# Kernel optimization log

Hardware: AMD Instinct MI355X
Metric: run time of the kernel (lower is better)

The kernel has to match this reference:

```python
import jax, jax.numpy as jnp
import numpy as np
import math

CH, CTX, NH, G = 512, 768, 8, 32
EPS = 1e-5

def setup_inputs() -> dict:
    key = jax.random.key(0)
    ks = jax.random.split(key, 12)
    s = 0.02
    return {
        "x": jax.random.normal(ks[0], (1, CH, 64, 64), dtype=jnp.float32),
        "context": jax.random.normal(ks[1], (1, CTX, 64, 64), dtype=jnp.float32),
        "gn_w": jnp.ones((CH,), jnp.float32),
        "gn_b": jnp.zeros((CH,), jnp.float32),
        "wq": jax.random.normal(ks[2], (CH, CH), jnp.float32) * s,
        "bq": jnp.zeros((CH,), jnp.float32),
        "wk": jax.random.normal(ks[3], (CH, CTX), jnp.float32) * s,
        "bk": jnp.zeros((CH,), jnp.float32),
        "wv": jax.random.normal(ks[4], (CH, CTX), jnp.float32) * s,
        "bv": jnp.zeros((CH,), jnp.float32),
        "wo": jax.random.normal(ks[5], (CH, CH), jnp.float32) * s,
        "bo": jnp.zeros((CH,), jnp.float32),
    }

def _group_norm(x, w, b):
    B, C, H, W = x.shape
    r = x.reshape(B, G, C // G, H, W)
    mu = jnp.mean(r, axis=(2, 3, 4), keepdims=True)
    var = jnp.var(r, axis=(2, 3, 4), keepdims=True)
    r = (r - mu) * jax.lax.rsqrt(var + EPS)
    return r.reshape(B, C, H, W) * w[None, :, None, None] + b[None, :, None, None]

def _conv1x1(x, w, b):
    # x: [B,Cin,H,W], w: [Cout,Cin]
    return jnp.einsum('bchw,oc->bohw', x, w) + b[None, :, None, None]

def reference(x, context, gn_w, gn_b, wq, bq, wk, bk, wv, bv, wo, bo):
    B, C, H, W = x.shape
    residual = x
    h = _group_norm(x, gn_w, gn_b)
    q = _conv1x1(h, wq, bq).reshape(B, NH, C // NH, H * W)
    k = _conv1x1(context, wk, bk).reshape(B, NH, C // NH, H * W)
    v = _conv1x1(context, wv, bv).reshape(B, NH, C // NH, H * W)
    scale = 1.0 / math.sqrt(C // NH)
    # chunked softmax in the original is mathematically exact full softmax
    attn = jnp.einsum('bhdi,bhdj->bhij', q, k) * scale
    attn = jax.nn.softmax(attn, axis=-1)
    out = jnp.einsum('bhij,bhdj->bhdi', attn, v).reshape(B, C, H, W)
    out = _conv1x1(out, wo, bo)
    return out + residual
```

## Files before the change

kernel.cpp:

```cpp
#include <hip/hip_runtime.h>
#include <cstdint>
#include <cstddef>

typedef __attribute__((ext_vector_type(8))) short bf16x8;
typedef __attribute__((ext_vector_type(4))) float f32x4;
typedef unsigned short u16;

#define QSCALE (0.125f * 1.44269504088896f)

__device__ inline u16 f2bf(float x) {
  uint32_t u = __builtin_bit_cast(uint32_t, x);
  u += 0x7FFFu + ((u >> 16) & 1u);
  return (u16)(u >> 16);
}
__device__ inline float bf2f(u16 v) {
  return __builtin_bit_cast(float, (uint32_t)v << 16);
}
__device__ inline uint32_t cvtpk(float a, float b) {
  uint32_t r;
  asm("v_cvt_pk_bf16_f32 %0, %1, %2" : "=v"(r) : "v"(a), "v"(b));
  return r;
}
__device__ inline float exp2raw(float x) {
  float r;
  asm("v_exp_f32 %0, %1" : "=v"(r) : "v"(x));
  return r;
}
__device__ inline void gload_lds16(const void* g, void* l) {
  __builtin_amdgcn_global_load_lds(
      (const __attribute__((address_space(1))) char*)g,
      (__attribute__((address_space(3))) char*)l, 16, 0, 0);
}

__global__ __launch_bounds__(256) void gn_partial(const float* __restrict__ x,
                                                  float* __restrict__ gsum,
                                                  float* __restrict__ gsum2) {
  __shared__ float rs[4], rss[4];
  int b = blockIdx.x;
  int g = b >> 3, sl = b & 7;
  const float* base = x + (size_t)g * 65536 + sl * 8192;
  int t = threadIdx.x;
  float s = 0.f, ss = 0.f;
#pragma unroll
  for (int i = 0; i < 8; ++i) {
    float4 v = *reinterpret_cast<const float4*>(base + i * 1024 + t * 4);
    s += v.x + v.y + v.z + v.w;
    ss += v.x * v.x + v.y * v.y + v.z * v.z + v.w * v.w;
  }
  for (int d = 32; d; d >>= 1) {
    s += __shfl_down(s, d, 64);
    ss += __shfl_down(ss, d, 64);
  }
  int wid = t >> 6;
  if ((t & 63) == 0) { rs[wid] = s; rss[wid] = ss; }
  __syncthreads();
  if (t == 0) {
    atomicAdd(gsum + g, rs[0] + rs[1] + rs[2] + rs[3]);
    atomicAdd(gsum2 + g, rss[0] + rss[1] + rss[2] + rss[3]);
  }
}

__global__ __launch_bounds__(256) void prep(const float* __restrict__ wq, u16* __restrict__ wqB,
                                            const float* __restrict__ wk, u16* __restrict__ wkB,
                                            const float* __restrict__ wv, u16* __restrict__ wvB,
                                            const float* __restrict__ wo, u16* __restrict__ woB,
                                            const float* __restrict__ x, u16* __restrict__ hT,
                                            const float* __restrict__ ctx, u16* __restrict__ ctxT,
                                            const float* __restrict__ gnw, const float* __restrict__ gnb,
                                            const float* __restrict__ gsum, const float* __restrict__ gsum2) {
  int b = blockIdx.x;
  int t = threadIdx.x;
  if (b < 1280) {
    const float* s; u16* d; int off;
    if (b < 256)       { s = wq; d = wqB; off = b; }
    else if (b < 640)  { s = wk; d = wkB; off = b - 256; }
    else if (b < 1024) { s = wv; d = wvB; off = b - 640; }
    else               { s = wo; d = woB; off = b - 1024; }
    int i = (off * 256 + t) * 4;
    float4 v = *reinterpret_cast<const float4*>(s + i);
    u16 o[4] = {f2bf(v.x), f2bf(v.y), f2bf(v.z), f2bf(v.w)};
    *reinterpret_cast<uint2*>(d + i) = *reinterpret_cast<const uint2*>(o);
    return;
  }
  __shared__ float tile[64][65];
  const float* in; u16* out; int C, p0, c0;
  bool norm = false;
  if (b < 1792) {
    int idx = b - 1280;
    in = x; out = hT; C = 512; p0 = (idx & 63) * 64; c0 = (idx >> 6) * 64; norm = true;
  } else {
    int idx = b - 1792;
    in = ctx; out = ctxT; C = 768; p0 = (idx & 63) * 64; c0 = (idx >> 6) * 64;
  }
  int cl = t >> 4, pl = (t & 15) * 4;
#pragma unroll
  for (int rep = 0; rep < 4; ++rep) {
    int c = cl + rep * 16;
    float4 v = *reinterpret_cast<const float4*>(in + (size_t)(c0 + c) * 4096 + p0 + pl);
    float s = 1.f, f = 0.f;
    if (norm) {
      int g = (c0 + c) >> 4;
      float mu = gsum[g] * (1.f / 65536.f);
      float var = gsum2[g] * (1.f / 65536.f) - mu * mu;
      float rstd = rsqrtf(var + 1e-5f);
      s = gnw[c0 + c] * rstd;
      f = gnb[c0 + c] - mu * s;
    }
    tile[c][pl + 0] = v.x * s + f;
    tile[c][pl + 1] = v.y * s + f;
    tile[c][pl + 2] = v.z * s + f;
    tile[c][pl + 3] = v.w * s + f;
  }
  __syncthreads();
#pragma unroll
  for (int rep = 0; rep < 16; ++rep) {
    int idx = rep * 256 + t;
    int pw = idx >> 6, cw = idx & 63;
    out[(size_t)(p0 + pw) * C + c0 + cw] = f2bf(tile[cw][pw]);
  }
}

template <int BIAS_MODE, bool OUT_BF16, bool ADD_RES>
__device__ inline void gemm_body(u16* __restrict__ aT, u16* __restrict__ bT,
                                 const u16* __restrict__ A, const u16* __restrict__ B,
                                 void* __restrict__ Dv,
                                 const float* __restrict__ bias,
                                 const float* __restrict__ res,
                                 int Rb, int K, float oscale, int bx, int by) {
  const int t = threadIdx.x;
  const int lane = t & 63, w = t >> 6;
  const int wr = w >> 1, wc = w & 1;
  const int l15 = lane & 15, l4 = lane >> 4;
  const int i0 = by * 128, j0 = bx * 64;
  const int r_st = t >> 3, slot = t & 7;
  f32x4 acc[4][2] = {};

  auto stage = [&](int kt, int b) {
#pragma unroll
    for (int q = 0; q < 4; ++q) {
      int row = q * 32 + r_st;
      int koff = kt + ((slot ^ (row & 7)) * 8);
      gload_lds16(A + (size_t)(i0 + row) * K + koff, (char*)aT + b * 16384 + q * 4096 + w * 1024);
    }
#pragma unroll
    for (int q = 0; q < 2; ++q) {
      int row = q * 32 + r_st;
      int koff = kt + ((slot ^ (row & 7)) * 8);
      gload_lds16(B + (size_t)(j0 + row) * K + koff, (char*)bT + b * 8192 + q * 4096 + w * 1024);
    }
  };

  const int nt = K / 64;
  stage(0, 0);
  stage(64, 1);

  for (int tt = 0; tt < nt; ++tt) {
    const int cur = tt % 3;
    if (tt + 1 < nt) asm volatile("s_waitcnt vmcnt(6)\n\ts_barrier" ::: "memory");
    else             asm volatile("s_waitcnt vmcnt(0)\n\ts_barrier" ::: "memory");
    if (tt + 2 < nt) stage((tt + 2) * 64, (tt + 2) % 3);

#pragma unroll
    for (int kk = 0; kk < 2; ++kk) {
      bf16x8 af[4], bfr[2];
#pragma unroll
      for (int m = 0; m < 4; ++m) {
        int row = wr * 64 + m * 16 + l15;
        int off = row * 128 + ((l4 * 16 + kk * 64) ^ ((row & 7) << 4));
        af[m] = *reinterpret_cast<const bf16x8*>((const char*)aT + cur * 16384 + off);
      }
#pragma unroll
      for (int n = 0; n < 2; ++n) {
        int row = wc * 32 + n * 16 + l15;
        int off = row * 128 + ((l4 * 16 + kk * 64) ^ ((row & 7) << 4));
        bfr[n] = *reinterpret_cast<const bf16x8*>((const char*)bT + cur * 8192 + off);
      }
#pragma unroll
      for (int m = 0; m < 4; ++m)
#pragma unroll
        for (int n = 0; n < 2; ++n)
          acc[m][n] = __builtin_amdgcn_mfma_f32_16x16x32_bf16(af[m], bfr[n], acc[m][n], 0, 0, 0);
    }
  }

#pragma unroll
  for (int m = 0; m < 4; ++m) {
    int ib = i0 + wr * 64 + m * 16 + l4 * 4;
#pragma unroll
    for (int n = 0; n < 2; ++n) {
      int j = j0 + wc * 32 + n * 16 + l15;
#pragma unroll
      for (int r = 0; r < 4; ++r) {
        int i = ib + r;
        float v = acc[m][n][r];
        if (BIAS_MODE == 0) v += bias[i];
        else v += bias[j];
        v *= oscale;
        if (ADD_RES) v += res[(size_t)i * Rb + j];
        if (OUT_BF16)
          ((u16*)Dv)[(size_t)i * Rb + j] = f2bf(v);
        else
          ((float*)Dv)[(size_t)i * Rb + j] = v;
      }
    }
  }
}

__global__ __launch_bounds__(256) void gemm_all(const u16* __restrict__ hT, const u16* __restrict__ ctxT,
                                                const u16* __restrict__ wqB, const u16* __restrict__ wkB,
                                                const u16* __restrict__ wvB,
                                                u16* __restrict__ QT, u16* __restrict__ KT, u16* __restrict__ Vb,
                                                const float* __restrict__ bq, const float* __restrict__ bk,
                                                const float* __restrict__ bv) {
  __shared__ u16 aT[3][128 * 64];
  __shared__ u16 bT[3][64 * 64];
  int b = blockIdx.x;
  if (b < 256)
    gemm_body<1, true, false>(&aT[0][0], &bT[0][0], hT, wqB, QT, bq, nullptr, 512, 512, QSCALE, b & 7, b >> 3);
  else if (b < 512)
    gemm_body<1, true, false>(&aT[0][0], &bT[0][0], ctxT, wkB, KT, bk, nullptr, 512, 768, 1.0f, (b - 256) & 7, (b - 256) >> 3);
  else
    gemm_body<0, true, false>(&aT[0][0], &bT[0][0], wvB, ctxT, Vb, bv, nullptr, 4096, 768, 1.0f, (b - 512) & 63, (b - 512) >> 6);
}

__global__ __launch_bounds__(256) void gemm_proj(const u16* __restrict__ woB, const u16* __restrict__ OtT,
                                                 void* __restrict__ Dv, const float* __restrict__ bo,
                                                 const float* __restrict__ res) {
  __shared__ u16 aT[3][128 * 64];
  __shared__ u16 bT[3][64 * 64];
  gemm_body<0, false, true>(&aT[0][0], &bT[0][0], woB, OtT, Dv, bo, res, 4096, 512, 1.0f,
                            blockIdx.x & 63, blockIdx.x >> 6);
}

__global__ __launch_bounds__(256) void attn_kernel(const u16* __restrict__ QT,
                                                   const u16* __restrict__ KT,
                                                   const u16* __restrict__ V,
                                                   u16* __restrict__ OpA,
                                                   u16* __restrict__ OpB,
                                                   float* __restrict__ Lb) {
  __shared__ u16 kbuf[2][64 * 64];
  __shared__ u16 vbuf[2][64 * 64];
  const int t = threadIdx.x;
  const int lane = t & 63, w = t >> 6;
  const int l15 = lane & 15, l4 = lane >> 4;
  int id = blockIdx.x;
  id = (id & 7) * 128 + (id >> 3);
  const int z = id >> 8;
  const int h = (id >> 5) & 7;
  const int q0 = (id & 31) * 128;
  const int tile0 = z * 16;
  const int r_st = t >> 3, slot = t & 7;

  bf16x8 qa[2][2];
#pragma unroll
  for (int f = 0; f < 2; ++f) {
    int qrow = q0 + w * 32 + f * 16 + l15;
    qa[f][0] = *reinterpret_cast<const bf16x8*>(QT + (size_t)qrow * 512 + h * 64 + l4 * 8);
    qa[f][1] = *reinterpret_cast<const bf16x8*>(QT + (size_t)qrow * 512 + h * 64 + 32 + l4 * 8);
  }

  f32x4 o0[4] = {}, o1[4] = {};
  f32x4 la0 = {}, la1 = {};
  const short oneb = (short)0x3F80;
  const bf16x8 ones = {oneb, oneb, oneb, oneb, oneb, oneb, oneb, oneb};

  int off0[4], off1[4];
#pragma unroll
  for (int n = 0; n < 4; ++n) {
    int row = n * 16 + l15, sw = (row & 7) << 4;
    off0[n] = row * 128 + ((l4 * 16) ^ sw);
    off1[n] = row * 128 + ((l4 * 16 + 64) ^ sw);
  }

  auto stageK = [&](int tile, int b) {
#pragma unroll
    for (int q = 0; q < 2; ++q) {
      int row = q * 32 + r_st;
      int so = (slot ^ (row & 7)) * 8;
      gload_lds16(KT + (size_t)(tile * 64 + row) * 512 + h * 64 + so,
                  (char*)kbuf[b] + q * 4096 + w * 1024);
    }
  };
  auto stageV = [&](int tile, int b) {
#pragma unroll
    for (int q = 0; q < 2; ++q) {
      int row = q * 32 + r_st;
      int so = ((((slot & 1) * 4 + (slot >> 1)) ^ (row & 7)) * 8);
      gload_lds16(V + (size_t)(h * 64 + row) * 4096 + tile * 64 + so,
                  (char*)vbuf[b] + q * 4096 + w * 1024);
    }
  };

  stageK(tile0, 0);
  stageV(tile0, 0);

#pragma unroll 2
  for (int kt = 0; kt < 16; ++kt) {
    const int cur = kt & 1;
    asm volatile("s_waitcnt vmcnt(0)\n\ts_barrier" ::: "memory");
    if (kt + 1 < 16) { stageK(tile0 + kt + 1, cur ^ 1); stageV(tile0 + kt + 1, cur ^ 1); }

    f32x4 s0[4], s1[4];
#pragma unroll
    for (int n = 0; n < 4; ++n) {
      bf16x8 kb0 = *reinterpret_cast<const bf16x8*>((const char*)kbuf[cur] + off0[n]);
      bf16x8 kb1 = *reinterpret_cast<const bf16x8*>((const char*)kbuf[cur] + off1[n]);
      f32x4 za = {};
      za = __builtin_amdgcn_mfma_f32_16x16x32_bf16(kb0, qa[0][0], za, 0, 0, 0);
      za = __builtin_amdgcn_mfma_f32_16x16x32_bf16(kb1, qa[0][1], za, 0, 0, 0);
      s0[n] = za;
      f32x4 zb = {};
      zb = __builtin_amdgcn_mfma_f32_16x16x32_bf16(kb0, qa[1][0], zb, 0, 0, 0);
      zb = __builtin_amdgcn_mfma_f32_16x16x32_bf16(kb1, qa[1][1], zb, 0, 0, 0);
      s1[n] = zb;
    }

#pragma unroll
    for (int n = 0; n < 4; ++n)
#pragma unroll
      for (int r = 0; r < 4; ++r) {
        s0[n][r] = exp2raw(s0[n][r]);
        s1[n][r] = exp2raw(s1[n][r]);
      }

    bf16x8 pa[2][2];
    {
      uint32_t u00 = cvtpk(s0[0][0], s0[0][1]), u01 = cvtpk(s0[0][2], s0[0][3]);
      uint32_t u10 = cvtpk(s0[1][0], s0[1][1]), u11 = cvtpk(s0[1][2], s0[1][3]);
      uint32_t u20 = cvtpk(s0[2][0], s0[2][1]), u21 = cvtpk(s0[2][2], s0[2][3]);
      uint32_t u30 = cvtpk(s0[3][0], s0[3][1]), u31 = cvtpk(s0[3][2], s0[3][3]);
      asm volatile("v_permlane16_swap_b32 %0, %1" : "+v"(u00), "+v"(u20));
      asm volatile("v_permlane16_swap_b32 %0, %1" : "+v"(u01), "+v"(u21));
      asm volatile("v_permlane16_swap_b32 %0, %1" : "+v"(u10), "+v"(u30));
      asm volatile("v_permlane16_swap_b32 %0, %1" : "+v"(u11), "+v"(u31));
      int4 p0i = {(int)u00, (int)u01, (int)u20, (int)u21};
      int4 p1i = {(int)u10, (int)u11, (int)u30, (int)u31};
      pa[0][0] = __builtin_bit_cast(bf16x8, p0i);
      pa[0][1] = __builtin_bit_cast(bf16x8, p1i);
    }
    {
      uint32_t u00 = cvtpk(s1[0][0], s1[0][1]), u01 = cvtpk(s1[0][2], s1[0][3]);
      uint32_t u10 = cvtpk(s1[1][0], s1[1][1]), u11 = cvtpk(s1[1][2], s1[1][3]);
      uint32_t u20 = cvtpk(s1[2][0], s1[2][1]), u21 = cvtpk(s1[2][2], s1[2][3]);
      uint32_t u30 = cvtpk(s1[3][0], s1[3][1]), u31 = cvtpk(s1[3][2], s1[3][3]);
      asm volatile("v_permlane16_swap_b32 %0, %1" : "+v"(u00), "+v"(u20));
      asm volatile("v_permlane16_swap_b32 %0, %1" : "+v"(u01), "+v"(u21));
      asm volatile("v_permlane16_swap_b32 %0, %1" : "+v"(u10), "+v"(u30));
      asm volatile("v_permlane16_swap_b32 %0, %1" : "+v"(u11), "+v"(u31));
      int4 p0i = {(int)u00, (int)u01, (int)u20, (int)u21};
      int4 p1i = {(int)u10, (int)u11, (int)u30, (int)u31};
      pa[1][0] = __builtin_bit_cast(bf16x8, p0i);
      pa[1][1] = __builtin_bit_cast(bf16x8, p1i);
    }

    la0 = __builtin_amdgcn_mfma_f32_16x16x32_bf16(pa[0][0], ones, la0, 0, 0, 0);
    la0 = __builtin_amdgcn_mfma_f32_16x16x32_bf16(pa[0][1], ones, la0, 0, 0, 0);
    la1 = __builtin_amdgcn_mfma_f32_16x16x32_bf16(pa[1][0], ones, la1, 0, 0, 0);
    la1 = __builtin_amdgcn_mfma_f32_16x16x32_bf16(pa[1][1], ones, la1, 0, 0, 0);

#pragma unroll
    for (int dt = 0; dt < 4; ++dt) {
      bf16x8 vb0 = *reinterpret_cast<const bf16x8*>((const char*)vbuf[cur] + off0[dt]);
      bf16x8 vb1 = *reinterpret_cast<const bf16x8*>((const char*)vbuf[cur] + off1[dt]);
      o0[dt] = __builtin_amdgcn_mfma_f32_16x16x32_bf16(pa[0][0], vb0, o0[dt], 0, 0, 0);
      o0[dt] = __builtin_amdgcn_mfma_f32_16x16x32_bf16(pa[0][1], vb1, o0[dt], 0, 0, 0);
      o1[dt] = __builtin_amdgcn_mfma_f32_16x16x32_bf16(pa[1][0], vb0, o1[dt], 0, 0, 0);
      o1[dt] = __builtin_amdgcn_mfma_f32_16x16x32_bf16(pa[1][1], vb1, o1[dt], 0, 0, 0);
    }
  }

  u16* obase = (z < 2) ? (OpA + (size_t)z * 4096 * 512) : (OpB + (size_t)(z - 2) * 4096 * 512);
#pragma unroll
  for (int r = 0; r < 4; ++r) {
    int orow0 = q0 + w * 32 + l4 * 4 + r;
#pragma unroll
    for (int dt = 0; dt < 4; ++dt) {
      obase[(size_t)orow0 * 512 + h * 64 + dt * 16 + l15] = f2bf(o0[dt][r]);
      obase[(size_t)(orow0 + 16) * 512 + h * 64 + dt * 16 + l15] = f2bf(o1[dt][r]);
    }
  }
  if (l15 == 0) {
    int q = q0 + w * 32 + l4 * 4;
#pragma unroll
    for (int r = 0; r < 4; ++r) {
      Lb[z * 32768 + h * 4096 + q + r] = la0[r];
      Lb[z * 32768 + h * 4096 + q + r + 16] = la1[r];
    }
  }
}

__global__ __launch_bounds__(256) void attn_combine(const u16* __restrict__ OpA,
                                                    const u16* __restrict__ OpB,
                                                    const float* __restrict__ Lb,
                                                    u16* __restrict__ OtT) {
  int idx = blockIdx.x * 256 + threadIdx.x;
  int q = idx >> 7;
  int c = (idx & 127) * 4;
  int h = c >> 6;
  float den = Lb[h * 4096 + q] + Lb[32768 + h * 4096 + q] +
              Lb[2 * 32768 + h * 4096 + q] + Lb[3 * 32768 + h * 4096 + q];
  float inv = 1.f / den;

  float acc[4] = {0.f, 0.f, 0.f, 0.f};
#pragma unroll
  for (int z = 0; z < 4; ++z) {
    const u16* base = (z < 2) ? (OpA + (size_t)z * 4096 * 512) : (OpB + (size_t)(z - 2) * 4096 * 512);
    uint2 a = *reinterpret_cast<const uint2*>(base + (size_t)q * 512 + c);
    acc[0] += bf2f((u16)(a.x & 0xFFFF));
    acc[1] += bf2f((u16)(a.x >> 16));
    acc[2] += bf2f((u16)(a.y & 0xFFFF));
    acc[3] += bf2f((u16)(a.y >> 16));
  }
  u16 o[4] = {f2bf(acc[0] * inv), f2bf(acc[1] * inv), f2bf(acc[2] * inv), f2bf(acc[3] * inv)};
  *reinterpret_cast<uint2*>(OtT + (size_t)q * 512 + c) = *reinterpret_cast<const uint2*>(o);
}

extern "C" void kernel_launch(void* const* d_in, const int* in_sizes, int n_in,
                              void* d_out, int out_size, void* d_ws, size_t ws_size,
                              hipStream_t stream) {
  const float* x    = (const float*)d_in[0];
  const float* ctx  = (const float*)d_in[1];
  const float* gn_w = (const float*)d_in[2];
  const float* gn_b = (const float*)d_in[3];
  const float* wq   = (const float*)d_in[4];
  const float* bq   = (const float*)d_in[5];
  const float* wk   = (const float*)d_in[6];
  const float* bk   = (const float*)d_in[7];
  const float* wv   = (const float*)d_in[8];
  const float* bv   = (const float*)d_in[9];
  const float* wo   = (const float*)d_in[10];
  const float* bo   = (const float*)d_in[11];

  char* ws = (char*)d_ws;
  float* gsum  = (float*)ws;
  float* gsum2 = gsum + 32;
  u16* woB    = (u16*)(ws + 4096);
  u16* wqB    = woB + 512 * 512;
  u16* wkB    = wqB + 512 * 512;
  u16* wvB    = wkB + 512 * 768;
  u16* hT     = wvB + 512 * 768;
  u16* ctxT   = hT + 4096 * 512;
  u16* QT     = ctxT + 4096 * 768;
  u16* KT     = QT + 4096 * 512;
  u16* Vb     = KT + 4096 * 512;
  u16* OtT    = Vb + (size_t)512 * 4096;
  float* Lb   = (float*)(OtT + (size_t)4096 * 512);
  u16* OpA    = wqB;
  u16* OpB    = (u16*)d_out;

  (void)hipMemsetAsync(gsum, 0, 256, stream);
  gn_partial<<<256, 256, 0, stream>>>(x, gsum, gsum2);
  prep<<<2560, 256, 0, stream>>>(wq, wqB, wk, wkB, wv, wvB, wo, woB,
                                 x, hT, ctx, ctxT, gn_w, gn_b, gsum, gsum2);

  gemm_all<<<768, 256, 0, stream>>>(hT, ctxT, wqB, wkB, wvB, QT, KT, Vb, bq, bk, bv);

  attn_kernel<<<1024, 256, 0, stream>>>(QT, KT, Vb, OpA, OpB, Lb);
  attn_combine<<<2048, 256, 0, stream>>>(OpA, OpB, Lb, OtT);

  gemm_proj<<<256, 256, 0, stream>>>(woB, OtT, (float*)d_out, bo, x);
}
```

Measured before the change: 103.9 us.

## Fuse attention split-combine into output projection GEMM and drop GN atomics

Removes the separate attn_combine kernel. The output-projection GEMM now loads the four bf16 partial attention outputs directly, sums them, scales by the reciprocal of the summed softmax denominators and writes the result into LDS as the B operand. This avoids writing and re-reading the combined OtT tensor and saves one kernel launch. The GroupNorm statistics path also drops the memset and atomics: per-block partial sums are written out and reduced in prep. In exchange the projection GEMM's B-operand staging now goes through registers with extra ALU work, where it previously used async LDS loads.

```diff
diff --git a/kernel.cpp b/kernel.cpp
--- a/kernel.cpp
+++ b/kernel.cpp
@@ -33,8 +33,8 @@
 }
 
 __global__ __launch_bounds__(256) void gn_partial(const float* __restrict__ x,
-                                                  float* __restrict__ gsum,
-                                                  float* __restrict__ gsum2) {
+                                                  float* __restrict__ gpart,
+                                                  float* __restrict__ gpart2) {
   __shared__ float rs[4], rss[4];
   int b = blockIdx.x;
   int g = b >> 3, sl = b & 7;
@@ -55,8 +55,8 @@
   if ((t & 63) == 0) { rs[wid] = s; rss[wid] = ss; }
   __syncthreads();
   if (t == 0) {
-    atomicAdd(gsum + g, rs[0] + rs[1] + rs[2] + rs[3]);
-    atomicAdd(gsum2 + g, rss[0] + rss[1] + rss[2] + rss[3]);
+    gpart[b] = rs[0] + rs[1] + rs[2] + rs[3];
+    gpart2[b] = rss[0] + rss[1] + rss[2] + rss[3];
   }
 }
 
@@ -67,7 +67,7 @@
                                             const float* __restrict__ x, u16* __restrict__ hT,
                                             const float* __restrict__ ctx, u16* __restrict__ ctxT,
                                             const float* __restrict__ gnw, const float* __restrict__ gnb,
-                                            const float* __restrict__ gsum, const float* __restrict__ gsum2) {
+                                            const float* __restrict__ gpart, const float* __restrict__ gpart2) {
   int b = blockIdx.x;
   int t = threadIdx.x;
   if (b < 1280) {
@@ -83,6 +83,7 @@
     return;
   }
   __shared__ float tile[64][65];
+  __shared__ float smu[4], srs[4];
   const float* in; u16* out; int C, p0, c0;
   bool norm = false;
   if (b < 1792) {
@@ -92,6 +93,22 @@
     int idx = b - 1792;
     in = ctx; out = ctxT; C = 768; p0 = (idx & 63) * 64; c0 = (idx >> 6) * 64;
   }
+  if (norm) {
+    if (t < 4) {
+      int g = (c0 >> 4) + t;
+      float S = 0.f, SS = 0.f;
+#pragma unroll
+      for (int sIdx = 0; sIdx < 8; ++sIdx) {
+        S += gpart[g * 8 + sIdx];
+        SS += gpart2[g * 8 + sIdx];
+      }
+      float mu = S * (1.f / 65536.f);
+      float var = SS * (1.f / 65536.f) - mu * mu;
+      smu[t] = mu;
+      srs[t] = rsqrtf(var + 1e-5f);
+    }
+    __syncthreads();
+  }
   int cl = t >> 4, pl = (t & 15) * 4;
 #pragma unroll
   for (int rep = 0; rep < 4; ++rep) {
@@ -99,12 +116,8 @@
     float4 v = *reinterpret_cast<const float4*>(in + (size_t)(c0 + c) * 4096 + p0 + pl);
     float s = 1.f, f = 0.f;
     if (norm) {
-      int g = (c0 + c) >> 4;
-      float mu = gsum[g] * (1.f / 65536.f);
-      float var = gsum2[g] * (1.f / 65536.f) - mu * mu;
-      float rstd = rsqrtf(var + 1e-5f);
-      s = gnw[c0 + c] * rstd;
-      f = gnb[c0 + c] - mu * s;
+      s = gnw[c0 + c] * srs[rep];
+      f = gnb[c0 + c] - smu[rep] * s;
     }
     tile[c][pl + 0] = v.x * s + f;
     tile[c][pl + 1] = v.y * s + f;
@@ -120,12 +133,11 @@
   }
 }
 
-template <int BIAS_MODE, bool OUT_BF16, bool ADD_RES>
+template <int BIAS_MODE>
 __device__ inline void gemm_body(u16* __restrict__ aT, u16* __restrict__ bT,
                                  const u16* __restrict__ A, const u16* __restrict__ B,
-                                 void* __restrict__ Dv,
+                                 u16* __restrict__ Dv,
                                  const float* __restrict__ bias,
-                                 const float* __restrict__ res,
                                  int Rb, int K, float oscale, int bx, int by) {
   const int t = threadIdx.x;
   const int lane = t & 63, w = t >> 6;
@@ -196,11 +208,7 @@
         if (BIAS_MODE == 0) v += bias[i];
         else v += bias[j];
         v *= oscale;
-        if (ADD_RES) v += res[(size_t)i * Rb + j];
-        if (OUT_BF16)
-          ((u16*)Dv)[(size_t)i * Rb + j] = f2bf(v);
-        else
-          ((float*)Dv)[(size_t)i * Rb + j] = v;
+        Dv[(size_t)i * Rb + j] = f2bf(v);
       }
     }
   }
@@ -216,27 +224,150 @@
   __shared__ u16 bT[3][64 * 64];
   int b = blockIdx.x;
   if (b < 256)
-    gemm_body<1, true, false>(&aT[0][0], &bT[0][0], hT, wqB, QT, bq, nullptr, 512, 512, QSCALE, b & 7, b >> 3);
+    gemm_body<1>(&aT[0][0], &bT[0][0], hT, wqB, QT, bq, 512, 512, QSCALE, b & 7, b >> 3);
   else if (b < 512)
-    gemm_body<1, true, false>(&aT[0][0], &bT[0][0], ctxT, wkB, KT, bk, nullptr, 512, 768, 1.0f, (b - 256) & 7, (b - 256) >> 3);
+    gemm_body<1>(&aT[0][0], &bT[0][0], ctxT, wkB, KT, bk, 512, 768, 1.0f, (b - 256) & 7, (b - 256) >> 3);
   else
-    gemm_body<0, true, false>(&aT[0][0], &bT[0][0], wvB, ctxT, Vb, bv, nullptr, 4096, 768, 1.0f, (b - 512) & 63, (b - 512) >> 6);
-}
-
-__global__ __launch_bounds__(256) void gemm_proj(const u16* __restrict__ woB, const u16* __restrict__ OtT,
-                                                 void* __restrict__ Dv, const float* __restrict__ bo,
-                                                 const float* __restrict__ res) {
+    gemm_body<0>(&aT[0][0], &bT[0][0], wvB, ctxT, Vb, bv, 4096, 768, 1.0f, (b - 512) & 63, (b - 512) >> 6);
+}
+
+__global__ __launch_bounds__(256) void gemm_projF(const u16* __restrict__ woB,
+                                                  const u16* __restrict__ P0, const u16* __restrict__ P1,
+                                                  const u16* __restrict__ P2, const u16* __restrict__ P3,
+                                                  const float* __restrict__ Lb,
+                                                  float* __restrict__ D, const float* __restrict__ bo,
+                                                  const float* __restrict__ res) {
   __shared__ u16 aT[3][128 * 64];
-  __shared__ u16 bT[3][64 * 64];
-  gemm_body<0, false, true>(&aT[0][0], &bT[0][0], woB, OtT, Dv, bo, res, 4096, 512, 1.0f,
-                            blockIdx.x & 63, blockIdx.x >> 6);
+  __shared__ u16 bT[2][64 * 64];
+  __shared__ float sinv[512];
+  const int t = threadIdx.x;
+  const int lane = t & 63, w = t >> 6;
+  const int wr = w >> 1, wc = w & 1;
+  const int l15 = lane & 15, l4 = lane >> 4;
+  const int bx = blockIdx.x & 63, by = blockIdx.x >> 6;
+  const int i0 = by * 128, j0 = bx * 64;
+  const int r_st = t >> 3, slot = t & 7;
+
+  {
+#pragma unroll
+    for (int r = 0; r < 2; ++r) {
+      int idx = t * 2 + r;
+      int hh = idx >> 6, jj = idx & 63;
+      int o = hh * 4096 + j0 + jj;
+      float den = Lb[o] + Lb[32768 + o] + Lb[65536 + o] + Lb[98304 + o];
+      sinv[idx] = 1.f / den;
+    }
+  }
+
+  auto stageA = [&](int kt, int b) {
+#pragma unroll
+    for (int q = 0; q < 4; ++q) {
+      int row = q * 32 + r_st;
+      int koff = kt + ((slot ^ (row & 7)) * 8);
+      gload_lds16(woB + (size_t)(i0 + row) * 512 + koff, (char*)aT + b * 16384 + q * 4096 + w * 1024);
+    }
+  };
+
+  const int brow = t >> 2;
+  const int bc0 = (t & 3) * 2;
+  uint4 rv[2][4];
+  auto loadB = [&](int kt) {
+#pragma unroll
+    for (int c = 0; c < 2; ++c) {
+      size_t off = (size_t)(j0 + brow) * 512 + kt + (bc0 + c) * 8;
+      rv[c][0] = *reinterpret_cast<const uint4*>(P0 + off);
+      rv[c][1] = *reinterpret_cast<const uint4*>(P1 + off);
+      rv[c][2] = *reinterpret_cast<const uint4*>(P2 + off);
+      rv[c][3] = *reinterpret_cast<const uint4*>(P3 + off);
+    }
+  };
+  auto writeB = [&](int kt, int buf) {
+    float inv = sinv[((kt >> 6) << 6) + brow];
+#pragma unroll
+    for (int c = 0; c < 2; ++c) {
+      uint32_t pk[4];
+#pragma unroll
+      for (int wi = 0; wi < 4; ++wi) {
+        uint32_t w0 = (wi == 0) ? rv[c][0].x : (wi == 1) ? rv[c][0].y : (wi == 2) ? rv[c][0].z : rv[c][0].w;
+        uint32_t w1 = (wi == 0) ? rv[c][1].x : (wi == 1) ? rv[c][1].y : (wi == 2) ? rv[c][1].z : rv[c][1].w;
+        uint32_t w2 = (wi == 0) ? rv[c][2].x : (wi == 1) ? rv[c][2].y : (wi == 2) ? rv[c][2].z : rv[c][2].w;
+        uint32_t w3 = (wi == 0) ? rv[c][3].x : (wi == 1) ? rv[c][3].y : (wi == 2) ? rv[c][3].z : rv[c][3].w;
+        float lo = __builtin_bit_cast(float, w0 << 16) + __builtin_bit_cast(float, w1 << 16) +
+                   __builtin_bit_cast(float, w2 << 16) + __builtin_bit_cast(float, w3 << 16);
+        float hi = __builtin_bit_cast(float, w0 & 0xFFFF0000u) + __builtin_bit_cast(float, w1 & 0xFFFF0000u) +
+                   __builtin_bit_cast(float, w2 & 0xFFFF0000u) + __builtin_bit_cast(float, w3 & 0xFFFF0000u);
+        pk[wi] = cvtpk(lo * inv, hi * inv);
+      }
+      uint4 outv = {pk[0], pk[1], pk[2], pk[3]};
+      int off = brow * 128 + (((bc0 + c) ^ (brow & 7)) * 16);
+      *reinterpret_cast<uint4*>((char*)&bT[buf][0] + off) = outv;
+    }
+  };
+
+  stageA(0, 0);
+  stageA(64, 1);
+  loadB(0);
+  asm volatile("s_waitcnt vmcnt(4)" ::: "memory");
+  writeB(0, 0);
+  asm volatile("s_waitcnt lgkmcnt(0)\n\ts_barrier" ::: "memory");
+
+  f32x4 acc[4][2] = {};
+  for (int tt = 0; tt < 8; ++tt) {
+    const int cur = tt & 1;
+    if (tt + 1 < 8) loadB((tt + 1) * 64);
+
+#pragma unroll
+    for (int kk = 0; kk < 2; ++kk) {
+      bf16x8 af[4], bfr[2];
+#pragma unroll
+      for (int m = 0; m < 4; ++m) {
+        int row = wr * 64 + m * 16 + l15;
+        int off = row * 128 + ((l4 * 16 + kk * 64) ^ ((row & 7) << 4));
+        af[m] = *reinterpret_cast<const bf16x8*>((const char*)aT + (tt % 3) * 16384 + off);
+      }
+#pragma unroll
+      for (int n = 0; n < 2; ++n) {
+        int row = wc * 32 + n * 16 + l15;
+        int off = row * 128 + ((l4 * 16 + kk * 64) ^ ((row & 7) << 4));
+        bfr[n] = *reinterpret_cast<const bf16x8*>((const char*)&bT[cur][0] + off);
+      }
+#pragma unroll
+      for (int m = 0; m < 4; ++m)
+#pragma unroll
+        for (int n = 0; n < 2; ++n)
+          acc[m][n] = __builtin_amdgcn_mfma_f32_16x16x32_bf16(af[m], bfr[n], acc[m][n], 0, 0, 0);
+    }
+
+    if (tt + 2 < 8) stageA((tt + 2) * 64, (tt + 2) % 3);
+    if (tt + 1 < 8) {
+      if (tt + 2 < 8) asm volatile("s_waitcnt vmcnt(4)" ::: "memory");
+      else            asm volatile("s_waitcnt vmcnt(0)" ::: "memory");
+      writeB((tt + 1) * 64, cur ^ 1);
+    }
+    asm volatile("s_waitcnt lgkmcnt(0)\n\ts_barrier" ::: "memory");
+  }
+
+#pragma unroll
+  for (int m = 0; m < 4; ++m) {
+    int ib = i0 + wr * 64 + m * 16 + l4 * 4;
+#pragma unroll
+    for (int n = 0; n < 2; ++n) {
+      int j = j0 + wc * 32 + n * 16 + l15;
+#pragma unroll
+      for (int r = 0; r < 4; ++r) {
+        int i = ib + r;
+        float v = acc[m][n][r] + bo[i] + res[(size_t)i * 4096 + j];
+        D[(size_t)i * 4096 + j] = v;
+      }
+    }
+  }
 }
 
 __global__ __launch_bounds__(256) void attn_kernel(const u16* __restrict__ QT,
                                                    const u16* __restrict__ KT,
                                                    const u16* __restrict__ V,
-                                                   u16* __restrict__ OpA,
-                                                   u16* __restrict__ OpB,
+                                                   u16* __restrict__ P0, u16* __restrict__ P1,
+                                                   u16* __restrict__ P2, u16* __restrict__ P3,
                                                    float* __restrict__ Lb) {
   __shared__ u16 kbuf[2][64 * 64];
   __shared__ u16 vbuf[2][64 * 64];
@@ -369,7 +500,7 @@
     }
   }
 
-  u16* obase = (z < 2) ? (OpA + (size_t)z * 4096 * 512) : (OpB + (size_t)(z - 2) * 4096 * 512);
+  u16* obase = (z == 0) ? P0 : (z == 1) ? P1 : (z == 2) ? P2 : P3;
 #pragma unroll
   for (int r = 0; r < 4; ++r) {
     int orow0 = q0 + w * 32 + l4 * 4 + r;
@@ -387,32 +518,6 @@
       Lb[z * 32768 + h * 4096 + q + r + 16] = la1[r];
     }
   }
-}
-
-__global__ __launch_bounds__(256) void attn_combine(const u16* __restrict__ OpA,
-                                                    const u16* __restrict__ OpB,
-                                                    const float* __restrict__ Lb,
-                                                    u16* __restrict__ OtT) {
-  int idx = blockIdx.x * 256 + threadIdx.x;
-  int q = idx >> 7;
-  int c = (idx & 127) * 4;
-  int h = c >> 6;
-  float den = Lb[h * 4096 + q] + Lb[32768 + h * 4096 + q] +
-              Lb[2 * 32768 + h * 4096 + q] + Lb[3 * 32768 + h * 4096 + q];
-  float inv = 1.f / den;
-
-  float acc[4] = {0.f, 0.f, 0.f, 0.f};
-#pragma unroll
-  for (int z = 0; z < 4; ++z) {
-    const u16* base = (z < 2) ? (OpA + (size_t)z * 4096 * 512) : (OpB + (size_t)(z - 2) * 4096 * 512);
-    uint2 a = *reinterpret_cast<const uint2*>(base + (size_t)q * 512 + c);
-    acc[0] += bf2f((u16)(a.x & 0xFFFF));
-    acc[1] += bf2f((u16)(a.x >> 16));
-    acc[2] += bf2f((u16)(a.y & 0xFFFF));
-    acc[3] += bf2f((u16)(a.y >> 16));
-  }
-  u16 o[4] = {f2bf(acc[0] * inv), f2bf(acc[1] * inv), f2bf(acc[2] * inv), f2bf(acc[3] * inv)};
-  *reinterpret_cast<uint2*>(OtT + (size_t)q * 512 + c) = *reinterpret_cast<const uint2*>(o);
 }
 
 extern "C" void kernel_launch(void* const* d_in, const int* in_sizes, int n_in,
@@ -432,8 +537,8 @@
   const float* bo   = (const float*)d_in[11];
 
   char* ws = (char*)d_ws;
-  float* gsum  = (float*)ws;
-  float* gsum2 = gsum + 32;
+  float* gpart  = (float*)ws;
+  float* gpart2 = gpart + 256;
   u16* woB    = (u16*)(ws + 4096);
   u16* wqB    = woB + 512 * 512;
   u16* wkB    = wqB + 512 * 512;
@@ -445,18 +550,18 @@
   u16* Vb     = KT + 4096 * 512;
   u16* OtT    = Vb + (size_t)512 * 4096;
   float* Lb   = (float*)(OtT + (size_t)4096 * 512);
-  u16* OpA    = wqB;
-  u16* OpB    = (u16*)d_out;
-
-  (void)hipMemsetAsync(gsum, 0, 256, stream);
-  gn_partial<<<256, 256, 0, stream>>>(x, gsum, gsum2);
+  u16* P0     = wqB;
+  u16* P1     = P0 + (size_t)4096 * 512;
+  u16* P2     = P1 + (size_t)4096 * 512;
+  u16* P3     = OtT;
+
+  gn_partial<<<256, 256, 0, stream>>>(x, gpart, gpart2);
   prep<<<2560, 256, 0, stream>>>(wq, wqB, wk, wkB, wv, wvB, wo, woB,
-                                 x, hT, ctx, ctxT, gn_w, gn_b, gsum, gsum2);
+                                 x, hT, ctx, ctxT, gn_w, gn_b, gpart, gpart2);
 
   gemm_all<<<768, 256, 0, stream>>>(hT, ctxT, wqB, wkB, wvB, QT, KT, Vb, bq, bk, bv);
 
-  attn_kernel<<<1024, 256, 0, stream>>>(QT, KT, Vb, OpA, OpB, Lb);
-  attn_combine<<<2048, 256, 0, stream>>>(OpA, OpB, Lb, OtT);
-
-  gemm_proj<<<256, 256, 0, stream>>>(woB, OtT, (float*)d_out, bo, x);
-}
+  attn_kernel<<<1024, 256, 0, stream>>>(QT, KT, Vb, P0, P1, P2, P3, Lb);
+
+  gemm_projF<<<256, 256, 0, stream>>>(woB, P0, P1, P2, P3, Lb, (float*)d_out, bo, x);
+}
```

Measured after the change: 96.47 us. -7.2%, faster.
